# Kernel tuning notes

Hardware: AMD Instinct MI355X
Metric: run time of the kernel (lower is better)

Reference implementation:

```python
import jax, jax.numpy as jnp
import numpy as np

N = 8192
D_IN = 64
D_OUT = 64
ALPHA = 0.2  # LeakyReLU negative slope


def setup_inputs() -> dict:
    key = jax.random.key(0)
    ks = jax.random.split(key, 6)
    s = 1.0 / np.sqrt(D_IN)
    return {
        "x": jax.random.normal(ks[0], (1, N, D_IN), dtype=jnp.float32),
        "Wt": jax.random.normal(ks[1], (D_IN, D_OUT), dtype=jnp.float32) * s,
        "a1": jax.random.normal(ks[2], (D_OUT,), dtype=jnp.float32) * s,
        "b1": jnp.zeros((), dtype=jnp.float32),
        "a2": jax.random.normal(ks[3], (D_OUT,), dtype=jnp.float32) * s,
        "b2": jnp.zeros((), dtype=jnp.float32),
    }


def reference(x, Wt, a1, b1, a2, b2):
    # Conv1d(kernel=1, bias=False) == pointwise linear: [1,N,Din] @ [Din,Dout]
    h = jnp.einsum("bni,io->bno", x, Wt)            # seq_fts, [1,N,Dout]
    f1 = jnp.einsum("bno,o->bn", h, a1) + b1        # per-node source score
    f2 = jnp.einsum("bno,o->bn", h, a2) + b2        # per-node target score
    logits = f1[:, :, None] + f2[:, None, :]        # [1,N,N]
    coefs = jax.nn.softmax(jax.nn.leaky_relu(logits, ALPHA), axis=-1)
    ret = jnp.einsum("bij,bjo->bio", coefs, h)      # [1,N,Dout]
    return jax.nn.elu(ret)                           # concat=True -> ELU
```

## Files before the change

kernel.cpp:

```cpp
#include <hip/hip_runtime.h>
#include <math.h>

#define N 8192
#define D 64
#define CHUNKS 512
#define CROWS 16
#define KS 32
#define SLICE 256
#define NQ (2 * N)

typedef unsigned long long u64;

__device__ __forceinline__ unsigned ordered_bits(float v) {
  unsigned u = __float_as_uint(v);
  return u ^ (((int)u >> 31) | 0x80000000u);
}

__global__ __launch_bounds__(256) void k1_gemm(
    const float* __restrict__ x, const float* __restrict__ Wt,
    const float* __restrict__ a1, const float* __restrict__ b1,
    const float* __restrict__ a2, const float* __restrict__ b2,
    float* __restrict__ h, float* __restrict__ f1, float* __restrict__ f2,
    u64* __restrict__ key64, u64* __restrict__ thrkey) {
  int t = threadIdx.x;
  int lane = t & 63, wv = t >> 6;
  float wcol[D];
#pragma unroll
  for (int k = 0; k < D; ++k) wcol[k] = Wt[k * D + lane];
  float a1d = a1[lane], a2d = a2[lane];
  float b1v = b1[0], b2v = b2[0];
  int rowBase = blockIdx.x * 16;
#pragma unroll
  for (int it = 0; it < 4; ++it) {
    int grow = rowBase + wv + it * 4;
    float xv = x[grow * D + lane];
    float acc = 0.f;
#pragma unroll
    for (int k = 0; k < D; ++k) acc += __shfl(xv, k) * wcol[k];
    h[grow * D + lane] = acc;
    float v1 = acc * a1d, v2 = acc * a2d;
#pragma unroll
    for (int off = 32; off > 0; off >>= 1) {
      v1 += __shfl_xor(v1, off);
      v2 += __shfl_xor(v2, off);
    }
    if (lane == 0) {
      float F1 = v1 + b1v, F2 = v2 + b2v;
      f1[grow] = F1;
      f2[grow] = F2;
      key64[grow] = ((u64)ordered_bits(F2) << 13) | (unsigned)grow;
      thrkey[grow] = ((u64)ordered_bits(-F1) << 13);
    }
  }
}

__global__ __launch_bounds__(256) void k2a_count(
    const u64* __restrict__ key64, const u64* __restrict__ thrkey,
    int* __restrict__ part) {
  __shared__ u64 ksl[SLICE];
  int t = threadIdx.x;
  int g = blockIdx.x >> 5;
  int s = blockIdx.x & (KS - 1);
  ksl[t] = key64[s * SLICE + t];
  int q0 = g * 1024 + t;
  u64 qa = (q0 < N) ? key64[q0] : thrkey[q0 - N];
  int q1 = q0 + 256;
  u64 qb = (q1 < N) ? key64[q1] : thrkey[q1 - N];
  int q2 = q0 + 512;
  u64 qc = (q2 < N) ? key64[q2] : thrkey[q2 - N];
  int q3 = q0 + 768;
  u64 qd = (q3 < N) ? key64[q3] : thrkey[q3 - N];
  __syncthreads();
  int c0 = 0, c1 = 0, c2 = 0, c3 = 0;
#pragma unroll 8
  for (int l = 0; l < SLICE; ++l) {
    u64 k = ksl[l];
    c0 += (k < qa) ? 1 : 0;
    c1 += (k < qb) ? 1 : 0;
    c2 += (k < qc) ? 1 : 0;
    c3 += (k < qd) ? 1 : 0;
  }
  int* pb = part + s * NQ;
  pb[q0] = c0;
  pb[q1] = c1;
  pb[q2] = c2;
  pb[q3] = c3;
}

__global__ __launch_bounds__(256) void k2b_reduce(
    const int* __restrict__ part, const float* __restrict__ f2,
    int* __restrict__ perm, float* __restrict__ wsm, float* __restrict__ wbg,
    int* __restrict__ ksplit) {
  int q = blockIdx.x * 256 + threadIdx.x;
  int tot = 0;
#pragma unroll
  for (int s = 0; s < KS; ++s) tot += part[s * NQ + q];
  if (q < N) {
    float v = f2[q];
    perm[tot] = q;
    wsm[tot] = expf(0.2f * v);
    wbg[tot] = expf(v);
  } else {
    ksplit[q - N] = tot;
  }
}

__global__ __launch_bounds__(256) void k3_scan(
    const float* __restrict__ h, const int* __restrict__ perm,
    const float* __restrict__ wsm, const float* __restrict__ wbg,
    float* __restrict__ Pl, float* __restrict__ Sl,
    float* __restrict__ pl, float* __restrict__ sl,
    float* __restrict__ tot_s, float* __restrict__ tot_b,
    float* __restrict__ tots_sc, float* __restrict__ totb_sc) {
  int t = threadIdx.x, lane = t & 63, wv = t >> 6;
  int c = blockIdx.x * 4 + wv;
  int base = c * CROWS;
  int dd = lane;
  int pj = (dd < CROWS) ? perm[base + dd] : 0;
  float wS = (dd < CROWS) ? wsm[base + dd] : 0.f;
  float wB = (dd < CROWS) ? wbg[base + dd] : 0.f;
  float hv[CROWS];
#pragma unroll
  for (int r = 0; r < CROWS; ++r) {
    int j = __shfl(pj, r);
    hv[r] = h[(size_t)j * D + dd];
  }
  float incS = wS, incB = wB;
#pragma unroll
  for (int off = 1; off < CROWS; off <<= 1) {
    float uS = __shfl_up(incS, off);
    float uB = __shfl_up(incB, off);
    if (dd >= off) { incS += uS; incB += uB; }
  }
  float totS = __shfl(incS, CROWS - 1);
  float totB = __shfl(incB, CROWS - 1);
  if (dd < CROWS) {
    pl[base + dd] = incS - wS;
    sl[base + dd] = totB - (incB - wB);
  }
  if (dd == 0) { tots_sc[c] = totS; totb_sc[c] = totB; }
  float runP = 0.f;
#pragma unroll
  for (int r = 0; r < CROWS; ++r) {
    Pl[(size_t)(base + r) * D + dd] = runP;
    runP += __shfl(wS, r) * hv[r];
  }
  tot_s[c * D + dd] = runP;
  float runS = 0.f;
#pragma unroll
  for (int r = CROWS - 1; r >= 0; --r) {
    runS += __shfl(wB, r) * hv[r];
    Sl[(size_t)(base + r) * D + dd] = runS;
  }
  tot_b[c * D + dd] = runS;
}

__global__ __launch_bounds__(512) void k3b_offsets(
    const float* __restrict__ tot_s, const float* __restrict__ tot_b,
    const float* __restrict__ tots_sc, const float* __restrict__ totb_sc,
    float* __restrict__ off_s, float* __restrict__ off_b,
    float* __restrict__ poff, float* __restrict__ soff,
    float* __restrict__ Pl, float* __restrict__ Sl,
    float* __restrict__ pl, float* __restrict__ sl) {
  __shared__ float sc[512];
  int t = threadIdx.x;
  int blk = blockIdx.x;
  if (blk < 64) {
    int dd = blk;
    float v = tot_s[t * D + dd];
    sc[t] = v;
    __syncthreads();
    float inc = v;
#pragma unroll
    for (int off = 1; off < 512; off <<= 1) {
      float u_ = (t >= off) ? sc[t - off] : 0.f;
      __syncthreads();
      inc += u_;
      sc[t] = inc;
      __syncthreads();
    }
    off_s[t * D + dd] = inc - v;
    if (t == 511) off_s[CHUNKS * D + dd] = inc;
    if (t == 0) Pl[(size_t)N * D + dd] = 0.f;
  } else if (blk < 128) {
    int dd = blk - 64;
    int rc = 511 - t;
    float v = tot_b[rc * D + dd];
    sc[t] = v;
    __syncthreads();
    float inc = v;
#pragma unroll
    for (int off = 1; off < 512; off <<= 1) {
      float u_ = (t >= off) ? sc[t - off] : 0.f;
      __syncthreads();
      inc += u_;
      sc[t] = inc;
      __syncthreads();
    }
    off_b[rc * D + dd] = inc - v;
    if (t == 0) {
      off_b[CHUNKS * D + dd] = 0.f;
      Sl[(size_t)N * D + dd] = 0.f;
    }
  } else {
    {
      float v = tots_sc[t];
      sc[t] = v;
      __syncthreads();
      float inc = v;
#pragma unroll
      for (int off = 1; off < 512; off <<= 1) {
        float u_ = (t >= off) ? sc[t - off] : 0.f;
        __syncthreads();
        inc += u_;
        sc[t] = inc;
        __syncthreads();
      }
      poff[t] = inc - v;
      if (t == 511) poff[CHUNKS] = inc;
      if (t == 0) pl[N] = 0.f;
    }
    __syncthreads();
    {
      int rc = 511 - t;
      float v = totb_sc[rc];
      sc[t] = v;
      __syncthreads();
      float inc = v;
#pragma unroll
      for (int off = 1; off < 512; off <<= 1) {
        float u_ = (t >= off) ? sc[t - off] : 0.f;
        __syncthreads();
        inc += u_;
        sc[t] = inc;
        __syncthreads();
      }
      soff[rc] = inc - v;
      if (t == 0) {
        soff[CHUNKS] = 0.f;
        sl[N] = 0.f;
      }
    }
  }
}

__global__ __launch_bounds__(256) void k4_out(
    const float* __restrict__ f1, const int* __restrict__ ksplit,
    const float* __restrict__ off_s, const float* __restrict__ off_b,
    const float* __restrict__ poff, const float* __restrict__ soff,
    const float* __restrict__ Pl, const float* __restrict__ Sl,
    const float* __restrict__ pl, const float* __restrict__ sl,
    float* __restrict__ out) {
  int g = blockIdx.x * 256 + threadIdx.x;
  int row = g >> 6, dd = g & 63;
  float f1v = f1[row];
  int k = ksplit[row];
  int c = k >> 4;
  float e1 = expf(f1v), e2 = expf(0.2f * f1v);
  float Sv = off_b[c * D + dd] + Sl[(size_t)k * D + dd];
  float Pv = off_s[c * D + dd] + Pl[(size_t)k * D + dd];
  float num = e1 * Sv + e2 * Pv;
  float den = e1 * (soff[c] + sl[k]) + e2 * (poff[c] + pl[k]);
  float v = num / den;
  out[g] = v > 0.f ? v : expm1f(v);
}

extern "C" void kernel_launch(void* const* d_in, const int* in_sizes, int n_in,
                              void* d_out, int out_size, void* d_ws,
                              size_t ws_size, hipStream_t stream) {
  const float* x = (const float*)d_in[0];
  const float* Wt = (const float*)d_in[1];
  const float* a1 = (const float*)d_in[2];
  const float* b1 = (const float*)d_in[3];
  const float* a2 = (const float*)d_in[4];
  const float* b2 = (const float*)d_in[5];
  float* out = (float*)d_out;

  u64* key64 = (u64*)d_ws;
  u64* thrkey = key64 + N;
  float* ws = (float*)(thrkey + N);
  float* h = ws;          ws += N * D;
  float* f1 = ws;         ws += N;
  float* f2v = ws;        ws += N;
  float* wsm = ws;        ws += N;
  float* wbg = ws;        ws += N;
  int* perm = (int*)ws;   ws += N;
  int* ksplit = (int*)ws; ws += N;
  int* part = (int*)ws;   ws += KS * NQ;
  float* Pl = ws;         ws += (size_t)(N + 1) * D;
  float* Sl = ws;         ws += (size_t)(N + 1) * D;
  float* tot_s = ws;      ws += CHUNKS * D;
  float* tot_b = ws;      ws += CHUNKS * D;
  float* off_s = ws;      ws += (CHUNKS + 1) * D;
  float* off_b = ws;      ws += (CHUNKS + 1) * D;
  float* pl = ws;         ws += (N + 1);
  float* sl = ws;         ws += (N + 1);
  float* tots_sc = ws;    ws += CHUNKS;
  float* totb_sc = ws;    ws += CHUNKS;
  float* poff = ws;       ws += (CHUNKS + 1);
  float* soff = ws;       ws += (CHUNKS + 1);

  k1_gemm<<<N / 16, 256, 0, stream>>>(x, Wt, a1, b1, a2, b2, h, f1, f2v,
                                      key64, thrkey);
  k2a_count<<<16 * KS, 256, 0, stream>>>(key64, thrkey, part);
  k2b_reduce<<<NQ / 256, 256, 0, stream>>>(part, f2v, perm, wsm, wbg, ksplit);
  k3_scan<<<CHUNKS / 4, 256, 0, stream>>>(h, perm, wsm, wbg, Pl, Sl, pl, sl,
                                          tot_s, tot_b, tots_sc, totb_sc);
  k3b_offsets<<<129, 512, 0, stream>>>(tot_s, tot_b, tots_sc, totb_sc, off_s,
                                       off_b, poff, soff, Pl, Sl, pl, sl);
  k4_out<<<(N * D) / 256, 256, 0, stream>>>(f1, ksplit, off_s, off_b, poff,
                                            soff, Pl, Sl, pl, sl, out);
}
```

Measured before the change: 98.79 us.

## Fuse all stages into one persistent kernel with atomic grid barriers

Merges the six launches (GEMM, rank count, reduce, chunk scan, offset scan, output) into one persistent kernel of 256 blocks, separated by software grid barriers built on atomics. The rank counting now has each block stage all keys in shared memory, and four threads per query count a quarter each, which removes the partial-count buffer and its reduction. This is meant to cut launch and inter-kernel gaps. In exchange it depends on all 256 blocks being co-resident, adds a memset and spin-wait barriers, and leaves many threads idle in the scan phases.

```diff
diff --git a/kernel.cpp b/kernel.cpp
--- a/kernel.cpp
+++ b/kernel.cpp
@@ -5,9 +5,9 @@
 #define D 64
 #define CHUNKS 512
 #define CROWS 16
-#define KS 32
-#define SLICE 256
 #define NQ (2 * N)
+#define NBLK 256
+#define NTHR 256
 
 typedef unsigned long long u64;
 
@@ -16,253 +16,234 @@
   return u ^ (((int)u >> 31) | 0x80000000u);
 }
 
-__global__ __launch_bounds__(256) void k1_gemm(
+__device__ __forceinline__ void gbar(int* bar) {
+  __syncthreads();
+  if (threadIdx.x == 0) {
+    __hip_atomic_fetch_add(bar, 1, __ATOMIC_ACQ_REL, __HIP_MEMORY_SCOPE_AGENT);
+    while (__hip_atomic_load(bar, __ATOMIC_ACQUIRE,
+                             __HIP_MEMORY_SCOPE_AGENT) < NBLK) {
+      __builtin_amdgcn_s_sleep(1);
+    }
+  }
+  __syncthreads();
+}
+
+__device__ __forceinline__ float hs_scan256(float s, float* sc, int t) {
+  sc[t] = s;
+  __syncthreads();
+  float inc = s;
+#pragma unroll
+  for (int off = 1; off < 256; off <<= 1) {
+    float u_ = (t >= off) ? sc[t - off] : 0.f;
+    __syncthreads();
+    inc += u_;
+    sc[t] = inc;
+    __syncthreads();
+  }
+  return inc;
+}
+
+__global__ __launch_bounds__(NTHR) void gat_fused(
     const float* __restrict__ x, const float* __restrict__ Wt,
     const float* __restrict__ a1, const float* __restrict__ b1,
     const float* __restrict__ a2, const float* __restrict__ b2,
     float* __restrict__ h, float* __restrict__ f1, float* __restrict__ f2,
-    u64* __restrict__ key64, u64* __restrict__ thrkey) {
-  int t = threadIdx.x;
-  int lane = t & 63, wv = t >> 6;
-  float wcol[D];
-#pragma unroll
-  for (int k = 0; k < D; ++k) wcol[k] = Wt[k * D + lane];
-  float a1d = a1[lane], a2d = a2[lane];
-  float b1v = b1[0], b2v = b2[0];
-  int rowBase = blockIdx.x * 16;
-#pragma unroll
-  for (int it = 0; it < 4; ++it) {
-    int grow = rowBase + wv + it * 4;
-    float xv = x[grow * D + lane];
-    float acc = 0.f;
-#pragma unroll
-    for (int k = 0; k < D; ++k) acc += __shfl(xv, k) * wcol[k];
-    h[grow * D + lane] = acc;
-    float v1 = acc * a1d, v2 = acc * a2d;
-#pragma unroll
-    for (int off = 32; off > 0; off >>= 1) {
-      v1 += __shfl_xor(v1, off);
-      v2 += __shfl_xor(v2, off);
-    }
-    if (lane == 0) {
-      float F1 = v1 + b1v, F2 = v2 + b2v;
-      f1[grow] = F1;
-      f2[grow] = F2;
-      key64[grow] = ((u64)ordered_bits(F2) << 13) | (unsigned)grow;
-      thrkey[grow] = ((u64)ordered_bits(-F1) << 13);
-    }
-  }
-}
-
-__global__ __launch_bounds__(256) void k2a_count(
-    const u64* __restrict__ key64, const u64* __restrict__ thrkey,
-    int* __restrict__ part) {
-  __shared__ u64 ksl[SLICE];
-  int t = threadIdx.x;
-  int g = blockIdx.x >> 5;
-  int s = blockIdx.x & (KS - 1);
-  ksl[t] = key64[s * SLICE + t];
-  int q0 = g * 1024 + t;
-  u64 qa = (q0 < N) ? key64[q0] : thrkey[q0 - N];
-  int q1 = q0 + 256;
-  u64 qb = (q1 < N) ? key64[q1] : thrkey[q1 - N];
-  int q2 = q0 + 512;
-  u64 qc = (q2 < N) ? key64[q2] : thrkey[q2 - N];
-  int q3 = q0 + 768;
-  u64 qd = (q3 < N) ? key64[q3] : thrkey[q3 - N];
-  __syncthreads();
-  int c0 = 0, c1 = 0, c2 = 0, c3 = 0;
-#pragma unroll 8
-  for (int l = 0; l < SLICE; ++l) {
-    u64 k = ksl[l];
-    c0 += (k < qa) ? 1 : 0;
-    c1 += (k < qb) ? 1 : 0;
-    c2 += (k < qc) ? 1 : 0;
-    c3 += (k < qd) ? 1 : 0;
-  }
-  int* pb = part + s * NQ;
-  pb[q0] = c0;
-  pb[q1] = c1;
-  pb[q2] = c2;
-  pb[q3] = c3;
-}
-
-__global__ __launch_bounds__(256) void k2b_reduce(
-    const int* __restrict__ part, const float* __restrict__ f2,
-    int* __restrict__ perm, float* __restrict__ wsm, float* __restrict__ wbg,
-    int* __restrict__ ksplit) {
-  int q = blockIdx.x * 256 + threadIdx.x;
-  int tot = 0;
-#pragma unroll
-  for (int s = 0; s < KS; ++s) tot += part[s * NQ + q];
-  if (q < N) {
-    float v = f2[q];
-    perm[tot] = q;
-    wsm[tot] = expf(0.2f * v);
-    wbg[tot] = expf(v);
-  } else {
-    ksplit[q - N] = tot;
-  }
-}
-
-__global__ __launch_bounds__(256) void k3_scan(
-    const float* __restrict__ h, const int* __restrict__ perm,
-    const float* __restrict__ wsm, const float* __restrict__ wbg,
-    float* __restrict__ Pl, float* __restrict__ Sl,
-    float* __restrict__ pl, float* __restrict__ sl,
-    float* __restrict__ tot_s, float* __restrict__ tot_b,
-    float* __restrict__ tots_sc, float* __restrict__ totb_sc) {
-  int t = threadIdx.x, lane = t & 63, wv = t >> 6;
-  int c = blockIdx.x * 4 + wv;
-  int base = c * CROWS;
-  int dd = lane;
-  int pj = (dd < CROWS) ? perm[base + dd] : 0;
-  float wS = (dd < CROWS) ? wsm[base + dd] : 0.f;
-  float wB = (dd < CROWS) ? wbg[base + dd] : 0.f;
-  float hv[CROWS];
-#pragma unroll
-  for (int r = 0; r < CROWS; ++r) {
-    int j = __shfl(pj, r);
-    hv[r] = h[(size_t)j * D + dd];
-  }
-  float incS = wS, incB = wB;
-#pragma unroll
-  for (int off = 1; off < CROWS; off <<= 1) {
-    float uS = __shfl_up(incS, off);
-    float uB = __shfl_up(incB, off);
-    if (dd >= off) { incS += uS; incB += uB; }
-  }
-  float totS = __shfl(incS, CROWS - 1);
-  float totB = __shfl(incB, CROWS - 1);
-  if (dd < CROWS) {
-    pl[base + dd] = incS - wS;
-    sl[base + dd] = totB - (incB - wB);
-  }
-  if (dd == 0) { tots_sc[c] = totS; totb_sc[c] = totB; }
-  float runP = 0.f;
-#pragma unroll
-  for (int r = 0; r < CROWS; ++r) {
-    Pl[(size_t)(base + r) * D + dd] = runP;
-    runP += __shfl(wS, r) * hv[r];
-  }
-  tot_s[c * D + dd] = runP;
-  float runS = 0.f;
-#pragma unroll
-  for (int r = CROWS - 1; r >= 0; --r) {
-    runS += __shfl(wB, r) * hv[r];
-    Sl[(size_t)(base + r) * D + dd] = runS;
-  }
-  tot_b[c * D + dd] = runS;
-}
-
-__global__ __launch_bounds__(512) void k3b_offsets(
-    const float* __restrict__ tot_s, const float* __restrict__ tot_b,
-    const float* __restrict__ tots_sc, const float* __restrict__ totb_sc,
-    float* __restrict__ off_s, float* __restrict__ off_b,
-    float* __restrict__ poff, float* __restrict__ soff,
-    float* __restrict__ Pl, float* __restrict__ Sl,
-    float* __restrict__ pl, float* __restrict__ sl) {
-  __shared__ float sc[512];
-  int t = threadIdx.x;
-  int blk = blockIdx.x;
-  if (blk < 64) {
-    int dd = blk;
-    float v = tot_s[t * D + dd];
-    sc[t] = v;
-    __syncthreads();
-    float inc = v;
-#pragma unroll
-    for (int off = 1; off < 512; off <<= 1) {
-      float u_ = (t >= off) ? sc[t - off] : 0.f;
+    u64* __restrict__ key64, u64* __restrict__ thrkey, int* __restrict__ perm,
+    float* __restrict__ wsm, float* __restrict__ wbg, int* __restrict__ ksplit,
+    float* __restrict__ Pl, float* __restrict__ Sl, float* __restrict__ pl,
+    float* __restrict__ sl, float* __restrict__ tot_s,
+    float* __restrict__ tot_b, float* __restrict__ tots_sc,
+    float* __restrict__ totb_sc, float* __restrict__ off_s,
+    float* __restrict__ off_b, float* __restrict__ poff,
+    float* __restrict__ soff, float* __restrict__ out, int* bars) {
+  __shared__ __align__(16) u64 ksl[4096];
+  const int t = threadIdx.x;
+  const int bid = blockIdx.x;
+  const int lane = t & 63, wv = t >> 6;
+
+  {
+    float wcol[D];
+#pragma unroll
+    for (int k = 0; k < D; ++k) wcol[k] = Wt[k * D + lane];
+    float a1d = a1[lane], a2d = a2[lane];
+    float b1v = b1[0], b2v = b2[0];
+    int rowBase = bid * 32;
+#pragma unroll
+    for (int it = 0; it < 8; ++it) {
+      int grow = rowBase + wv + it * 4;
+      float xv = x[grow * D + lane];
+      float acc = 0.f;
+#pragma unroll
+      for (int k = 0; k < D; ++k) acc += __shfl(xv, k) * wcol[k];
+      h[grow * D + lane] = acc;
+      float v1 = acc * a1d, v2 = acc * a2d;
+#pragma unroll
+      for (int off = 32; off > 0; off >>= 1) {
+        v1 += __shfl_xor(v1, off);
+        v2 += __shfl_xor(v2, off);
+      }
+      if (lane == 0) {
+        float F1 = v1 + b1v, F2 = v2 + b2v;
+        f1[grow] = F1;
+        f2[grow] = F2;
+        key64[grow] = ((u64)ordered_bits(F2) << 13) | (unsigned)grow;
+        thrkey[grow] = ((u64)ordered_bits(-F1) << 13);
+      }
+    }
+  }
+  gbar(bars + 0);
+
+  {
+    int q = bid * 64 + (t >> 2);
+    int sub = t & 3;
+    u64 qv = (q < N) ? key64[q] : thrkey[q - N];
+    int cnt = 0;
+#pragma unroll
+    for (int p = 0; p < 2; ++p) {
+      const u64* kp = key64 + p * 4096;
+#pragma unroll
+      for (int i = 0; i < 16; ++i) ksl[t + i * 256] = kp[t + i * 256];
       __syncthreads();
-      inc += u_;
-      sc[t] = inc;
+      const u64* kb = ksl + sub * 1024;
+#pragma unroll 4
+      for (int j = 0; j < 512; ++j) {
+        int jj = (j + sub) & 511;
+        u64 k0 = kb[2 * jj], k1 = kb[2 * jj + 1];
+        cnt += (k0 < qv) ? 1 : 0;
+        cnt += (k1 < qv) ? 1 : 0;
+      }
       __syncthreads();
     }
-    off_s[t * D + dd] = inc - v;
-    if (t == 511) off_s[CHUNKS * D + dd] = inc;
-    if (t == 0) Pl[(size_t)N * D + dd] = 0.f;
-  } else if (blk < 128) {
-    int dd = blk - 64;
-    int rc = 511 - t;
-    float v = tot_b[rc * D + dd];
-    sc[t] = v;
-    __syncthreads();
-    float inc = v;
-#pragma unroll
-    for (int off = 1; off < 512; off <<= 1) {
-      float u_ = (t >= off) ? sc[t - off] : 0.f;
-      __syncthreads();
-      inc += u_;
-      sc[t] = inc;
-      __syncthreads();
-    }
-    off_b[rc * D + dd] = inc - v;
-    if (t == 0) {
-      off_b[CHUNKS * D + dd] = 0.f;
-      Sl[(size_t)N * D + dd] = 0.f;
-    }
-  } else {
-    {
-      float v = tots_sc[t];
-      sc[t] = v;
-      __syncthreads();
-      float inc = v;
-#pragma unroll
-      for (int off = 1; off < 512; off <<= 1) {
-        float u_ = (t >= off) ? sc[t - off] : 0.f;
-        __syncthreads();
-        inc += u_;
-        sc[t] = inc;
-        __syncthreads();
-      }
-      poff[t] = inc - v;
-      if (t == 511) poff[CHUNKS] = inc;
+    cnt += __shfl_xor(cnt, 1);
+    cnt += __shfl_xor(cnt, 2);
+    if (sub == 0) {
+      if (q < N) {
+        float v = f2[q];
+        perm[cnt] = q;
+        wsm[cnt] = expf(0.2f * v);
+        wbg[cnt] = expf(v);
+      } else {
+        ksplit[q - N] = cnt;
+      }
+    }
+  }
+  gbar(bars + 1);
+
+  if (wv < 2) {
+    int c = bid * 2 + wv;
+    int base = c * CROWS;
+    int dd = lane;
+    int pj = (dd < CROWS) ? perm[base + dd] : 0;
+    float wS = (dd < CROWS) ? wsm[base + dd] : 0.f;
+    float wB = (dd < CROWS) ? wbg[base + dd] : 0.f;
+    float hv[CROWS];
+#pragma unroll
+    for (int r = 0; r < CROWS; ++r) {
+      int j = __shfl(pj, r);
+      hv[r] = h[(size_t)j * D + dd];
+    }
+    float incS = wS, incB = wB;
+#pragma unroll
+    for (int off = 1; off < CROWS; off <<= 1) {
+      float uS = __shfl_up(incS, off);
+      float uB = __shfl_up(incB, off);
+      if (dd >= off) { incS += uS; incB += uB; }
+    }
+    float totS = __shfl(incS, CROWS - 1);
+    float totB = __shfl(incB, CROWS - 1);
+    if (dd < CROWS) {
+      pl[base + dd] = incS - wS;
+      sl[base + dd] = totB - (incB - wB);
+    }
+    if (dd == 0) { tots_sc[c] = totS; totb_sc[c] = totB; }
+    float runP = 0.f;
+#pragma unroll
+    for (int r = 0; r < CROWS; ++r) {
+      Pl[(size_t)(base + r) * D + dd] = runP;
+      runP += __shfl(wS, r) * hv[r];
+    }
+    tot_s[c * D + dd] = runP;
+    float runS = 0.f;
+#pragma unroll
+    for (int r = CROWS - 1; r >= 0; --r) {
+      runS += __shfl(wB, r) * hv[r];
+      Sl[(size_t)(base + r) * D + dd] = runS;
+    }
+    tot_b[c * D + dd] = runS;
+  }
+  gbar(bars + 2);
+
+  {
+    float* sc = (float*)ksl;
+    int task = bid;
+    if (task < 64) {
+      int dd = task;
+      float a = tot_s[(size_t)(2 * t) * D + dd];
+      float b = tot_s[(size_t)(2 * t + 1) * D + dd];
+      float s = a + b;
+      float inc = hs_scan256(s, sc, t);
+      float ex = inc - s;
+      off_s[(2 * t) * D + dd] = ex;
+      off_s[(2 * t + 1) * D + dd] = ex + a;
+      if (t == 255) off_s[CHUNKS * D + dd] = inc;
+      if (t == 0) Pl[(size_t)N * D + dd] = 0.f;
+    } else if (task < 128) {
+      int dd = task - 64;
+      int c0 = 511 - 2 * t, c1 = 510 - 2 * t;
+      float a = tot_b[(size_t)c0 * D + dd];
+      float b = tot_b[(size_t)c1 * D + dd];
+      float s = a + b;
+      float inc = hs_scan256(s, sc, t);
+      float ex = inc - s;
+      off_b[c0 * D + dd] = ex;
+      off_b[c1 * D + dd] = ex + a;
+      if (t == 0) {
+        off_b[CHUNKS * D + dd] = 0.f;
+        Sl[(size_t)N * D + dd] = 0.f;
+      }
+    } else if (task == 128) {
+      float a = tots_sc[2 * t], b = tots_sc[2 * t + 1];
+      float s = a + b;
+      float inc = hs_scan256(s, sc, t);
+      float ex = inc - s;
+      poff[2 * t] = ex;
+      poff[2 * t + 1] = ex + a;
+      if (t == 255) poff[CHUNKS] = inc;
       if (t == 0) pl[N] = 0.f;
-    }
-    __syncthreads();
-    {
-      int rc = 511 - t;
-      float v = totb_sc[rc];
-      sc[t] = v;
-      __syncthreads();
-      float inc = v;
-#pragma unroll
-      for (int off = 1; off < 512; off <<= 1) {
-        float u_ = (t >= off) ? sc[t - off] : 0.f;
-        __syncthreads();
-        inc += u_;
-        sc[t] = inc;
-        __syncthreads();
-      }
-      soff[rc] = inc - v;
+    } else if (task == 129) {
+      int c0 = 511 - 2 * t, c1 = 510 - 2 * t;
+      float a = totb_sc[c0], b = totb_sc[c1];
+      float s = a + b;
+      float inc = hs_scan256(s, sc, t);
+      float ex = inc - s;
+      soff[c0] = ex;
+      soff[c1] = ex + a;
       if (t == 0) {
         soff[CHUNKS] = 0.f;
         sl[N] = 0.f;
       }
     }
   }
-}
-
-__global__ __launch_bounds__(256) void k4_out(
-    const float* __restrict__ f1, const int* __restrict__ ksplit,
-    const float* __restrict__ off_s, const float* __restrict__ off_b,
-    const float* __restrict__ poff, const float* __restrict__ soff,
-    const float* __restrict__ Pl, const float* __restrict__ Sl,
-    const float* __restrict__ pl, const float* __restrict__ sl,
-    float* __restrict__ out) {
-  int g = blockIdx.x * 256 + threadIdx.x;
-  int row = g >> 6, dd = g & 63;
-  float f1v = f1[row];
-  int k = ksplit[row];
-  int c = k >> 4;
-  float e1 = expf(f1v), e2 = expf(0.2f * f1v);
-  float Sv = off_b[c * D + dd] + Sl[(size_t)k * D + dd];
-  float Pv = off_s[c * D + dd] + Pl[(size_t)k * D + dd];
-  float num = e1 * Sv + e2 * Pv;
-  float den = e1 * (soff[c] + sl[k]) + e2 * (poff[c] + pl[k]);
-  float v = num / den;
-  out[g] = v > 0.f ? v : expm1f(v);
+  gbar(bars + 3);
+
+  {
+    int T = bid * NTHR + t;
+#pragma unroll
+    for (int p = 0; p < 8; ++p) {
+      int g = T + p * (NBLK * NTHR);
+      int row = g >> 6, dd = g & 63;
+      float f1v = f1[row];
+      int k = ksplit[row];
+      int c = k >> 4;
+      float e1 = expf(f1v), e2 = expf(0.2f * f1v);
+      float Sv = off_b[c * D + dd] + Sl[(size_t)k * D + dd];
+      float Pv = off_s[c * D + dd] + Pl[(size_t)k * D + dd];
+      float num = e1 * Sv + e2 * Pv;
+      float den = e1 * (soff[c] + sl[k]) + e2 * (poff[c] + pl[k]);
+      float v = num / den;
+      out[g] = v > 0.f ? v : expm1f(v);
+    }
+  }
 }
 
 extern "C" void kernel_launch(void* const* d_in, const int* in_sizes, int n_in,
@@ -276,7 +257,8 @@
   const float* b2 = (const float*)d_in[5];
   float* out = (float*)d_out;
 
-  u64* key64 = (u64*)d_ws;
+  int* bars = (int*)d_ws;
+  u64* key64 = (u64*)((char*)d_ws + 16);
   u64* thrkey = key64 + N;
   float* ws = (float*)(thrkey + N);
   float* h = ws;          ws += N * D;
@@ -286,7 +268,6 @@
   float* wbg = ws;        ws += N;
   int* perm = (int*)ws;   ws += N;
   int* ksplit = (int*)ws; ws += N;
-  int* part = (int*)ws;   ws += KS * NQ;
   float* Pl = ws;         ws += (size_t)(N + 1) * D;
   float* Sl = ws;         ws += (size_t)(N + 1) * D;
   float* tot_s = ws;      ws += CHUNKS * D;
@@ -300,14 +281,9 @@
   float* poff = ws;       ws += (CHUNKS + 1);
   float* soff = ws;       ws += (CHUNKS + 1);
 
-  k1_gemm<<<N / 16, 256, 0, stream>>>(x, Wt, a1, b1, a2, b2, h, f1, f2v,
-                                      key64, thrkey);
-  k2a_count<<<16 * KS, 256, 0, stream>>>(key64, thrkey, part);
-  k2b_reduce<<<NQ / 256, 256, 0, stream>>>(part, f2v, perm, wsm, wbg, ksplit);
-  k3_scan<<<CHUNKS / 4, 256, 0, stream>>>(h, perm, wsm, wbg, Pl, Sl, pl, sl,
-                                          tot_s, tot_b, tots_sc, totb_sc);
-  k3b_offsets<<<129, 512, 0, stream>>>(tot_s, tot_b, tots_sc, totb_sc, off_s,
-                                       off_b, poff, soff, Pl, Sl, pl, sl);
-  k4_out<<<(N * D) / 256, 256, 0, stream>>>(f1, ksplit, off_s, off_b, poff,
-                                            soff, Pl, Sl, pl, sl, out);
-}
+  hipMemsetAsync(bars, 0, 4 * sizeof(int), stream);
+  gat_fused<<<NBLK, NTHR, 0, stream>>>(
+      x, Wt, a1, b1, a2, b2, h, f1, f2v, key64, thrkey, perm, wsm, wbg,
+      ksplit, Pl, Sl, pl, sl, tot_s, tot_b, tots_sc, totb_sc, off_s, off_b,
+      poff, soff, out, bars);
+}
```

New measurement: 208.9 us. 111% more time.

## Fuse rank count with reduction and fold chunk-offset scan into output kernel

Applied to the files above, without the earlier changes.

Merges the partial-count and reduce kernels into one rank kernel in which each wave splits the key set across lanes and combines counts with shuffles. This removes the partial-count buffer and one launch. Drops the separate offsets-scan kernel: each output block recomputes chunk prefix and suffix sums over all 512 chunk totals and snapshots the values each of its rows needs. This cuts two launches and their serial dependencies, but every output block now reads all chunk totals again, which is redundant work.

```diff
diff --git a/kernel.cpp b/kernel.cpp
--- a/kernel.cpp
+++ b/kernel.cpp
@@ -5,8 +5,6 @@
 #define D 64
 #define CHUNKS 512
 #define CROWS 16
-#define KS 32
-#define SLICE 256
 #define NQ (2 * N)
 
 typedef unsigned long long u64;
@@ -54,54 +52,60 @@
   }
 }
 
-__global__ __launch_bounds__(256) void k2a_count(
+__global__ __launch_bounds__(256) void k2_rank(
     const u64* __restrict__ key64, const u64* __restrict__ thrkey,
-    int* __restrict__ part) {
-  __shared__ u64 ksl[SLICE];
+    const float* __restrict__ f2, int* __restrict__ perm,
+    float* __restrict__ wsm, float* __restrict__ wbg,
+    int* __restrict__ ksplit) {
+  __shared__ u64 ksl[4096];
   int t = threadIdx.x;
-  int g = blockIdx.x >> 5;
-  int s = blockIdx.x & (KS - 1);
-  ksl[t] = key64[s * SLICE + t];
-  int q0 = g * 1024 + t;
-  u64 qa = (q0 < N) ? key64[q0] : thrkey[q0 - N];
-  int q1 = q0 + 256;
-  u64 qb = (q1 < N) ? key64[q1] : thrkey[q1 - N];
-  int q2 = q0 + 512;
-  u64 qc = (q2 < N) ? key64[q2] : thrkey[q2 - N];
-  int q3 = q0 + 768;
-  u64 qd = (q3 < N) ? key64[q3] : thrkey[q3 - N];
-  __syncthreads();
-  int c0 = 0, c1 = 0, c2 = 0, c3 = 0;
+  int lane = t & 63, wv = t >> 6;
+  int q2 = lane & 1, s = lane >> 1;
+  int qbase = blockIdx.x * 32 + wv * 8 + q2 * 4;
+  u64 qv[4];
+#pragma unroll
+  for (int qi = 0; qi < 4; ++qi) {
+    int q = qbase + qi;
+    qv[qi] = (q < N) ? key64[q] : thrkey[q - N];
+  }
+  int cnt[4] = {0, 0, 0, 0};
+#pragma unroll
+  for (int p = 0; p < 2; ++p) {
+    const u64* kp = key64 + p * 4096;
+#pragma unroll
+    for (int i = 0; i < 16; ++i) ksl[t + i * 256] = kp[t + i * 256];
+    __syncthreads();
+    const u64* kb = ksl + s * 128;
 #pragma unroll 8
-  for (int l = 0; l < SLICE; ++l) {
-    u64 k = ksl[l];
-    c0 += (k < qa) ? 1 : 0;
-    c1 += (k < qb) ? 1 : 0;
-    c2 += (k < qc) ? 1 : 0;
-    c3 += (k < qd) ? 1 : 0;
-  }
-  int* pb = part + s * NQ;
-  pb[q0] = c0;
-  pb[q1] = c1;
-  pb[q2] = c2;
-  pb[q3] = c3;
-}
-
-__global__ __launch_bounds__(256) void k2b_reduce(
-    const int* __restrict__ part, const float* __restrict__ f2,
-    int* __restrict__ perm, float* __restrict__ wsm, float* __restrict__ wbg,
-    int* __restrict__ ksplit) {
-  int q = blockIdx.x * 256 + threadIdx.x;
-  int tot = 0;
-#pragma unroll
-  for (int s = 0; s < KS; ++s) tot += part[s * NQ + q];
-  if (q < N) {
-    float v = f2[q];
-    perm[tot] = q;
-    wsm[tot] = expf(0.2f * v);
-    wbg[tot] = expf(v);
-  } else {
-    ksplit[q - N] = tot;
+    for (int j = 0; j < 128; ++j) {
+      int jj = (j + s) & 127;
+      u64 k = kb[jj];
+      cnt[0] += (k < qv[0]) ? 1 : 0;
+      cnt[1] += (k < qv[1]) ? 1 : 0;
+      cnt[2] += (k < qv[2]) ? 1 : 0;
+      cnt[3] += (k < qv[3]) ? 1 : 0;
+    }
+    __syncthreads();
+  }
+#pragma unroll
+  for (int off = 2; off < 64; off <<= 1) {
+#pragma unroll
+    for (int qi = 0; qi < 4; ++qi) cnt[qi] += __shfl_xor(cnt[qi], off);
+  }
+  if (s == 0) {
+#pragma unroll
+    for (int qi = 0; qi < 4; ++qi) {
+      int q = qbase + qi;
+      int rank = cnt[qi];
+      if (q < N) {
+        float v = f2[q];
+        perm[rank] = q;
+        wsm[rank] = expf(0.2f * v);
+        wbg[rank] = expf(v);
+      } else {
+        ksplit[q - N] = rank;
+      }
+    }
   }
 }
 
@@ -153,116 +157,117 @@
     Sl[(size_t)(base + r) * D + dd] = runS;
   }
   tot_b[c * D + dd] = runS;
-}
-
-__global__ __launch_bounds__(512) void k3b_offsets(
+  if (c == CHUNKS - 1) {
+    Pl[(size_t)N * D + dd] = 0.f;
+    Sl[(size_t)N * D + dd] = 0.f;
+    if (dd == 0) { pl[N] = 0.f; sl[N] = 0.f; }
+  }
+}
+
+__global__ __launch_bounds__(256) void k4_out(
+    const float* __restrict__ f1, const int* __restrict__ ksplit,
     const float* __restrict__ tot_s, const float* __restrict__ tot_b,
     const float* __restrict__ tots_sc, const float* __restrict__ totb_sc,
-    float* __restrict__ off_s, float* __restrict__ off_b,
-    float* __restrict__ poff, float* __restrict__ soff,
-    float* __restrict__ Pl, float* __restrict__ Sl,
-    float* __restrict__ pl, float* __restrict__ sl) {
-  __shared__ float sc[512];
-  int t = threadIdx.x;
-  int blk = blockIdx.x;
-  if (blk < 64) {
-    int dd = blk;
-    float v = tot_s[t * D + dd];
-    sc[t] = v;
-    __syncthreads();
-    float inc = v;
-#pragma unroll
-    for (int off = 1; off < 512; off <<= 1) {
-      float u_ = (t >= off) ? sc[t - off] : 0.f;
-      __syncthreads();
-      inc += u_;
-      sc[t] = inc;
-      __syncthreads();
-    }
-    off_s[t * D + dd] = inc - v;
-    if (t == 511) off_s[CHUNKS * D + dd] = inc;
-    if (t == 0) Pl[(size_t)N * D + dd] = 0.f;
-  } else if (blk < 128) {
-    int dd = blk - 64;
-    int rc = 511 - t;
-    float v = tot_b[rc * D + dd];
-    sc[t] = v;
-    __syncthreads();
-    float inc = v;
-#pragma unroll
-    for (int off = 1; off < 512; off <<= 1) {
-      float u_ = (t >= off) ? sc[t - off] : 0.f;
-      __syncthreads();
-      inc += u_;
-      sc[t] = inc;
-      __syncthreads();
-    }
-    off_b[rc * D + dd] = inc - v;
-    if (t == 0) {
-      off_b[CHUNKS * D + dd] = 0.f;
-      Sl[(size_t)N * D + dd] = 0.f;
-    }
-  } else {
-    {
-      float v = tots_sc[t];
-      sc[t] = v;
-      __syncthreads();
-      float inc = v;
-#pragma unroll
-      for (int off = 1; off < 512; off <<= 1) {
-        float u_ = (t >= off) ? sc[t - off] : 0.f;
-        __syncthreads();
-        inc += u_;
-        sc[t] = inc;
-        __syncthreads();
-      }
-      poff[t] = inc - v;
-      if (t == 511) poff[CHUNKS] = inc;
-      if (t == 0) pl[N] = 0.f;
-    }
-    __syncthreads();
-    {
-      int rc = 511 - t;
-      float v = totb_sc[rc];
-      sc[t] = v;
-      __syncthreads();
-      float inc = v;
-#pragma unroll
-      for (int off = 1; off < 512; off <<= 1) {
-        float u_ = (t >= off) ? sc[t - off] : 0.f;
-        __syncthreads();
-        inc += u_;
-        sc[t] = inc;
-        __syncthreads();
-      }
-      soff[rc] = inc - v;
-      if (t == 0) {
-        soff[CHUNKS] = 0.f;
-        sl[N] = 0.f;
-      }
-    }
-  }
-}
-
-__global__ __launch_bounds__(256) void k4_out(
-    const float* __restrict__ f1, const int* __restrict__ ksplit,
-    const float* __restrict__ off_s, const float* __restrict__ off_b,
-    const float* __restrict__ poff, const float* __restrict__ soff,
     const float* __restrict__ Pl, const float* __restrict__ Sl,
     const float* __restrict__ pl, const float* __restrict__ sl,
     float* __restrict__ out) {
-  int g = blockIdx.x * 256 + threadIdx.x;
-  int row = g >> 6, dd = g & 63;
-  float f1v = f1[row];
-  int k = ksplit[row];
-  int c = k >> 4;
-  float e1 = expf(f1v), e2 = expf(0.2f * f1v);
-  float Sv = off_b[c * D + dd] + Sl[(size_t)k * D + dd];
-  float Pv = off_s[c * D + dd] + Pl[(size_t)k * D + dd];
-  float num = e1 * Sv + e2 * Pv;
-  float den = e1 * (soff[c] + sl[k]) + e2 * (poff[c] + pl[k]);
-  float v = num / den;
-  out[g] = v > 0.f ? v : expm1f(v);
+  __shared__ int sh_k[16];
+  __shared__ int sh_c[16];
+  __shared__ float sh_f1[16];
+  __shared__ unsigned map[CHUNKS];
+  __shared__ float segP[4][D], segB[4][D];
+  __shared__ float segPs[4], segBs[4];
+  __shared__ float snapP[16][D], snapS[16][D];
+  __shared__ float snapPs[16], snapSs[16];
+  int t = threadIdx.x;
+  int dd = t & 63, seg = t >> 6;
+  int r0 = blockIdx.x * 16;
+  map[t] = 0;
+  map[t + 256] = 0;
+  __syncthreads();
+  if (t < 16) {
+    int k = ksplit[r0 + t];
+    sh_k[t] = k;
+    int c = k >> 4;
+    sh_c[t] = c;
+    sh_f1[t] = f1[r0 + t];
+    if (c < CHUNKS) atomicOr(&map[c], 1u << t);
+  }
+  __syncthreads();
+  int cs = seg * 128;
+  float tP = 0.f, tB = 0.f, tPs = 0.f, tBs = 0.f;
+#pragma unroll 4
+  for (int j = 0; j < 128; ++j) {
+    int c = cs + j;
+    tP += tot_s[c * D + dd];
+    tB += tot_b[c * D + dd];
+    tPs += tots_sc[c];
+    tBs += totb_sc[c];
+  }
+  segP[seg][dd] = tP;
+  segB[seg][dd] = tB;
+  if (dd == 0) { segPs[seg] = tPs; segBs[seg] = tBs; }
+  __syncthreads();
+  float startP = 0.f, startPs = 0.f;
+  for (int s2 = 0; s2 < seg; ++s2) { startP += segP[s2][dd]; startPs += segPs[s2]; }
+  float startS = 0.f, startSs = 0.f;
+  for (int s2 = seg + 1; s2 < 4; ++s2) { startS += segB[s2][dd]; startSs += segBs[s2]; }
+  float grandP = segP[0][dd] + segP[1][dd] + segP[2][dd] + segP[3][dd];
+  float grandPs = segPs[0] + segPs[1] + segPs[2] + segPs[3];
+  float runP = startP, runPs = startPs;
+#pragma unroll 4
+  for (int j = 0; j < 128; ++j) {
+    int c = cs + j;
+    unsigned m = map[c];
+    while (m) {
+      int slot = __ffs(m) - 1;
+      m &= m - 1;
+      snapP[slot][dd] = runP;
+      if (dd == 0) snapPs[slot] = runPs;
+    }
+    runP += tot_s[c * D + dd];
+    runPs += tots_sc[c];
+  }
+  float runS = startS, runSs = startSs;
+#pragma unroll 4
+  for (int j = 0; j < 128; ++j) {
+    int c = cs + 127 - j;
+    unsigned m = map[c];
+    while (m) {
+      int slot = __ffs(m) - 1;
+      m &= m - 1;
+      snapS[slot][dd] = runS;
+      if (dd == 0) snapSs[slot] = runSs;
+    }
+    runS += tot_b[c * D + dd];
+    runSs += totb_sc[c];
+  }
+  __syncthreads();
+  if (seg == 0) {
+#pragma unroll
+    for (int slot = 0; slot < 16; ++slot) {
+      if (sh_c[slot] == CHUNKS) {
+        snapP[slot][dd] = grandP;
+        snapS[slot][dd] = 0.f;
+        if (dd == 0) { snapPs[slot] = grandPs; snapSs[slot] = 0.f; }
+      }
+    }
+  }
+  __syncthreads();
+#pragma unroll
+  for (int ii = 0; ii < 4; ++ii) {
+    int slot = seg * 4 + ii;
+    int row = r0 + slot;
+    int k = sh_k[slot];
+    float f1v = sh_f1[slot];
+    float e1 = expf(f1v), e2 = expf(0.2f * f1v);
+    float Pv = snapP[slot][dd] + Pl[(size_t)k * D + dd];
+    float Sv = snapS[slot][dd] + Sl[(size_t)k * D + dd];
+    float num = e1 * Sv + e2 * Pv;
+    float den = e1 * (snapSs[slot] + sl[k]) + e2 * (snapPs[slot] + pl[k]);
+    float v = num / den;
+    out[row * D + dd] = v > 0.f ? v : expm1f(v);
+  }
 }
 
 extern "C" void kernel_launch(void* const* d_in, const int* in_sizes, int n_in,
@@ -286,28 +291,21 @@
   float* wbg = ws;        ws += N;
   int* perm = (int*)ws;   ws += N;
   int* ksplit = (int*)ws; ws += N;
-  int* part = (int*)ws;   ws += KS * NQ;
   float* Pl = ws;         ws += (size_t)(N + 1) * D;
   float* Sl = ws;         ws += (size_t)(N + 1) * D;
   float* tot_s = ws;      ws += CHUNKS * D;
   float* tot_b = ws;      ws += CHUNKS * D;
-  float* off_s = ws;      ws += (CHUNKS + 1) * D;
-  float* off_b = ws;      ws += (CHUNKS + 1) * D;
   float* pl = ws;         ws += (N + 1);
   float* sl = ws;         ws += (N + 1);
   float* tots_sc = ws;    ws += CHUNKS;
   float* totb_sc = ws;    ws += CHUNKS;
-  float* poff = ws;       ws += (CHUNKS + 1);
-  float* soff = ws;       ws += (CHUNKS + 1);
 
   k1_gemm<<<N / 16, 256, 0, stream>>>(x, Wt, a1, b1, a2, b2, h, f1, f2v,
                                       key64, thrkey);
-  k2a_count<<<16 * KS, 256, 0, stream>>>(key64, thrkey, part);
-  k2b_reduce<<<NQ / 256, 256, 0, stream>>>(part, f2v, perm, wsm, wbg, ksplit);
+  k2_rank<<<NQ / 32, 256, 0, stream>>>(key64, thrkey, f2v, perm, wsm, wbg,
+                                       ksplit);
   k3_scan<<<CHUNKS / 4, 256, 0, stream>>>(h, perm, wsm, wbg, Pl, Sl, pl, sl,
                                           tot_s, tot_b, tots_sc, totb_sc);
-  k3b_offsets<<<129, 512, 0, stream>>>(tot_s, tot_b, tots_sc, totb_sc, off_s,
-                                       off_b, poff, soff, Pl, Sl, pl, sl);
-  k4_out<<<(N * D) / 256, 256, 0, stream>>>(f1, ksplit, off_s, off_b, poff,
-                                            soff, Pl, Sl, pl, sl, out);
-}
+  k4_out<<<N / 16, 256, 0, stream>>>(f1, ksplit, tot_s, tot_b, tots_sc,
+                                     totb_sc, Pl, Sl, pl, sl, out);
+}
```

After: 140.8 us. 42.5% more time.

## Fuse rank counting and reduction into a single kernel with in-wave shuffle reduce

Applied to the files above, without the earlier changes.

Replaces the two-kernel rank computation (per-slice partial counts written to global memory, then summed) with one kernel. Each block loads all 8192 keys into shared memory in two halves, each wave's lanes split the key range, and counts are combined with xor shuffles before perm, weights and split indices are written directly. This removes the partial-count buffer round trip and one launch. In exchange each block now reads the full key array, 512 blocks reload 64KB each, and shared memory use per block rises to 32KB.

```diff
diff --git a/kernel.cpp b/kernel.cpp
--- a/kernel.cpp
+++ b/kernel.cpp
@@ -5,8 +5,6 @@
 #define D 64
 #define CHUNKS 512
 #define CROWS 16
-#define KS 32
-#define SLICE 256
 #define NQ (2 * N)
 
 typedef unsigned long long u64;
@@ -54,54 +52,60 @@
   }
 }
 
-__global__ __launch_bounds__(256) void k2a_count(
+__global__ __launch_bounds__(256) void k2_rank(
     const u64* __restrict__ key64, const u64* __restrict__ thrkey,
-    int* __restrict__ part) {
-  __shared__ u64 ksl[SLICE];
+    const float* __restrict__ f2, int* __restrict__ perm,
+    float* __restrict__ wsm, float* __restrict__ wbg,
+    int* __restrict__ ksplit) {
+  __shared__ u64 ksl[4096];
   int t = threadIdx.x;
-  int g = blockIdx.x >> 5;
-  int s = blockIdx.x & (KS - 1);
-  ksl[t] = key64[s * SLICE + t];
-  int q0 = g * 1024 + t;
-  u64 qa = (q0 < N) ? key64[q0] : thrkey[q0 - N];
-  int q1 = q0 + 256;
-  u64 qb = (q1 < N) ? key64[q1] : thrkey[q1 - N];
-  int q2 = q0 + 512;
-  u64 qc = (q2 < N) ? key64[q2] : thrkey[q2 - N];
-  int q3 = q0 + 768;
-  u64 qd = (q3 < N) ? key64[q3] : thrkey[q3 - N];
-  __syncthreads();
-  int c0 = 0, c1 = 0, c2 = 0, c3 = 0;
+  int lane = t & 63, wv = t >> 6;
+  int q2 = lane & 1, s = lane >> 1;
+  int qbase = blockIdx.x * 32 + wv * 8 + q2 * 4;
+  u64 qv[4];
+#pragma unroll
+  for (int qi = 0; qi < 4; ++qi) {
+    int q = qbase + qi;
+    qv[qi] = (q < N) ? key64[q] : thrkey[q - N];
+  }
+  int cnt[4] = {0, 0, 0, 0};
+#pragma unroll
+  for (int p = 0; p < 2; ++p) {
+    const u64* kp = key64 + p * 4096;
+#pragma unroll
+    for (int i = 0; i < 16; ++i) ksl[t + i * 256] = kp[t + i * 256];
+    __syncthreads();
+    const u64* kb = ksl + s * 128;
 #pragma unroll 8
-  for (int l = 0; l < SLICE; ++l) {
-    u64 k = ksl[l];
-    c0 += (k < qa) ? 1 : 0;
-    c1 += (k < qb) ? 1 : 0;
-    c2 += (k < qc) ? 1 : 0;
-    c3 += (k < qd) ? 1 : 0;
-  }
-  int* pb = part + s * NQ;
-  pb[q0] = c0;
-  pb[q1] = c1;
-  pb[q2] = c2;
-  pb[q3] = c3;
-}
-
-__global__ __launch_bounds__(256) void k2b_reduce(
-    const int* __restrict__ part, const float* __restrict__ f2,
-    int* __restrict__ perm, float* __restrict__ wsm, float* __restrict__ wbg,
-    int* __restrict__ ksplit) {
-  int q = blockIdx.x * 256 + threadIdx.x;
-  int tot = 0;
-#pragma unroll
-  for (int s = 0; s < KS; ++s) tot += part[s * NQ + q];
-  if (q < N) {
-    float v = f2[q];
-    perm[tot] = q;
-    wsm[tot] = expf(0.2f * v);
-    wbg[tot] = expf(v);
-  } else {
-    ksplit[q - N] = tot;
+    for (int j = 0; j < 128; ++j) {
+      int jj = (j + s) & 127;
+      u64 k = kb[jj];
+      cnt[0] += (k < qv[0]) ? 1 : 0;
+      cnt[1] += (k < qv[1]) ? 1 : 0;
+      cnt[2] += (k < qv[2]) ? 1 : 0;
+      cnt[3] += (k < qv[3]) ? 1 : 0;
+    }
+    __syncthreads();
+  }
+#pragma unroll
+  for (int off = 2; off < 64; off <<= 1) {
+#pragma unroll
+    for (int qi = 0; qi < 4; ++qi) cnt[qi] += __shfl_xor(cnt[qi], off);
+  }
+  if (s == 0) {
+#pragma unroll
+    for (int qi = 0; qi < 4; ++qi) {
+      int q = qbase + qi;
+      int rank = cnt[qi];
+      if (q < N) {
+        float v = f2[q];
+        perm[rank] = q;
+        wsm[rank] = expf(0.2f * v);
+        wbg[rank] = expf(v);
+      } else {
+        ksplit[q - N] = rank;
+      }
+    }
   }
 }
 
@@ -286,7 +290,6 @@
   float* wbg = ws;        ws += N;
   int* perm = (int*)ws;   ws += N;
   int* ksplit = (int*)ws; ws += N;
-  int* part = (int*)ws;   ws += KS * NQ;
   float* Pl = ws;         ws += (size_t)(N + 1) * D;
   float* Sl = ws;         ws += (size_t)(N + 1) * D;
   float* tot_s = ws;      ws += CHUNKS * D;
@@ -302,8 +305,8 @@
 
   k1_gemm<<<N / 16, 256, 0, stream>>>(x, Wt, a1, b1, a2, b2, h, f1, f2v,
                                       key64, thrkey);
-  k2a_count<<<16 * KS, 256, 0, stream>>>(key64, thrkey, part);
-  k2b_reduce<<<NQ / 256, 256, 0, stream>>>(part, f2v, perm, wsm, wbg, ksplit);
+  k2_rank<<<NQ / 32, 256, 0, stream>>>(key64, thrkey, f2v, perm, wsm, wbg,
+                                       ksplit);
   k3_scan<<<CHUNKS / 4, 256, 0, stream>>>(h, perm, wsm, wbg, Pl, Sl, pl, sl,
                                           tot_s, tot_b, tots_sc, totb_sc);
   k3b_offsets<<<129, 512, 0, stream>>>(tot_s, tot_b, tots_sc, totb_sc, off_s,
```

After: 100.2 us. Within noise of the previous version (+1.5%).
